# Kernel optimization log

Hardware: AMD Instinct MI355X
Metric: run time of the kernel (lower is better)

Reference implementation:

```python
import jax, jax.numpy as jnp
from jax import lax
import numpy as np

B, T, N = 32, 1024, 128


def setup_inputs() -> dict:
    key = jax.random.key(0)
    k1, k2, k3 = jax.random.split(key, 3)
    x = jax.random.normal(k1, (B, T, N), dtype=jnp.float32)
    w_init = jax.random.normal(k2, (B, N, N), dtype=jnp.float32)
    mask = jax.random.randint(k3, (B, T), 0, 2, dtype=jnp.int32)
    alpha = jnp.float32(0.9)
    eta = jnp.float32(0.01)
    return {"x": x, "w_init": w_init, "alpha": alpha, "eta": eta, "mask": mask}


def reference(x, w_init, alpha, eta, mask):
    # x: (B,T,N), w_init: (B,N,N), mask: (B,T) int {0,1}
    maskf = mask.astype(x.dtype)

    def step(w, inp):
        xt, mt = inp                       # (B,N), (B,)
        yt = jnp.einsum('bij,bj->bi', w, xt)           # read-out with OLD w
        outer = xt[:, :, None] * xt[:, None, :]        # (B,N,N) Hebbian outer product
        w_new = alpha * w + eta * outer                # decay + Hebbian update
        m = mt[:, None, None]
        w = m * w_new + (1.0 - m) * w                  # masked update
        return w, yt

    xs = jnp.swapaxes(x, 0, 1)     # (T,B,N)
    ms = jnp.swapaxes(maskf, 0, 1) # (T,B)
    w_final, ys = lax.scan(step, w_init, (xs, ms))
    y_seq = jnp.swapaxes(ys, 0, 1)  # (B,T,N)
    return w_final, y_seq
```

## Files before the change

### kernel.cpp

```cpp
#include <hip/hip_runtime.h>

#define BB 32
#define TT 1024
#define NN 128
#define YB 256

#define ROR_ADD(p, ctrl)                                                      \
  p += __int_as_float(__builtin_amdgcn_update_dpp(                            \
      0, __float_as_int(p), ctrl, 0xF, 0xF, true));
#define BCAST15_ADD(p)                                                        \
  p += __int_as_float(__builtin_amdgcn_update_dpp(                            \
      0, __float_as_int(p), 0x142, 0xF, 0xF, true));

__global__ __launch_bounds__(256)
void bdh_seq_kernel(const float* __restrict__ x,
                    const float* __restrict__ w_init,
                    const float* __restrict__ alpha_p,
                    const float* __restrict__ eta_p,
                    const int*   __restrict__ mask,
                    float* __restrict__ out)
{
    const int tid  = threadIdx.x;
    const int bidx = blockIdx.x;
    const int b      = bidx & 31;
    const int i_base = (bidx >> 5) << 3;
    const int rloc   = tid >> 5;
    const int i      = i_base + rloc;
    const int cg     = tid & 31;
    const int j0     = cg << 2;

    __shared__ float ybuf[YB][8];

    const float alpha = alpha_p[0];
    const float eta   = eta_p[0];

    const float* xb = x + (size_t)b * TT * NN;
    const int*   mb = mask + b * TT;

    float* wout = out + ((size_t)b * NN + i) * NN + j0;
    float* yout = out + (size_t)BB * NN * NN + (size_t)b * TT * NN;

    float4 w = *reinterpret_cast<const float4*>(
        w_init + ((size_t)b * NN + i) * NN + j0);

    float4 Xc[8], Xn[8];
    float  xic[8], xin[8];
    int    mc[8],  mn[8];
    float  p[16];

#define LOADG(X, XI, M, tbase)                                                \
  {                                                                           \
    const float* gp = xb + (size_t)(tbase) * NN;                              \
    _Pragma("unroll")                                                         \
    for (int k = 0; k < 8; ++k) {                                             \
      X[k]  = *reinterpret_cast<const float4*>(gp + k * NN + j0);             \
      XI[k] = gp[k * NN + i];                                                 \
    }                                                                         \
    *reinterpret_cast<int4*>(&M[0]) =                                         \
        *reinterpret_cast<const int4*>(mb + (tbase));                         \
    *reinterpret_cast<int4*>(&M[4]) =                                         \
        *reinterpret_cast<const int4*>(mb + (tbase) + 4);                     \
  }

#define COMPG(X, XI, M, pbase)                                                \
  {                                                                           \
    _Pragma("unroll")                                                         \
    for (int k = 0; k < 8; ++k) {                                             \
      const float aa = M[k] ? alpha : 1.0f;                                   \
      const float ci = (M[k] ? eta : 0.0f) * XI[k];                           \
      float p0 = fmaf(w.y, X[k].y, w.x * X[k].x);                             \
      float p1 = fmaf(w.w, X[k].w, w.z * X[k].z);                             \
      p[(pbase) + k] = p0 + p1;                                               \
      w.x = fmaf(aa, w.x, ci * X[k].x);                                       \
      w.y = fmaf(aa, w.y, ci * X[k].y);                                       \
      w.z = fmaf(aa, w.z, ci * X[k].z);                                       \
      w.w = fmaf(aa, w.w, ci * X[k].w);                                       \
    }                                                                         \
  }

    LOADG(Xc, xic, mc, 0);
    LOADG(Xn, xin, mn, 8);

#pragma unroll 1
    for (int t = 0; t < TT; t += 16) {
        COMPG(Xc, xic, mc, 0);
        if (t + 16 < TT) LOADG(Xc, xic, mc, t + 16);
        COMPG(Xn, xin, mn, 8);
        if (t + 24 < TT) LOADG(Xn, xin, mn, t + 24);

#pragma unroll
        for (int k = 0; k < 16; ++k) { ROR_ADD(p[k], 0x121); }
#pragma unroll
        for (int k = 0; k < 16; ++k) { ROR_ADD(p[k], 0x122); }
#pragma unroll
        for (int k = 0; k < 16; ++k) { ROR_ADD(p[k], 0x124); }
#pragma unroll
        for (int k = 0; k < 16; ++k) { ROR_ADD(p[k], 0x128); }
#pragma unroll
        for (int k = 0; k < 16; ++k) { BCAST15_ADD(p[k]); }

        if (cg == 16) {
#pragma unroll
            for (int k = 0; k < 16; ++k)
                ybuf[(t + k) & (YB - 1)][rloc] = p[k];
        }

        if (((t + 16) & (YB - 1)) == 0) {
            __syncthreads();
            const int t0 = t + 16 - YB;
#pragma unroll
            for (int pass = 0; pass < 8; ++pass) {
                const int tq = (tid >> 3) + (pass << 5);
                const int il = tid & 7;
                yout[(size_t)(t0 + tq) * NN + i_base + il] = ybuf[tq][il];
            }
            __syncthreads();
        }
    }
#undef LOADG
#undef COMPG

    *reinterpret_cast<float4*>(wout) = w;
}

extern "C" void kernel_launch(void* const* d_in, const int* in_sizes, int n_in,
                              void* d_out, int out_size, void* d_ws, size_t ws_size,
                              hipStream_t stream)
{
    const float* x      = (const float*)d_in[0];
    const float* w_init = (const float*)d_in[1];
    const float* alpha  = (const float*)d_in[2];
    const float* eta    = (const float*)d_in[3];
    const int*   mask   = (const int*)d_in[4];
    float*       out    = (float*)d_out;

    dim3 grid(512), block(256);
    hipLaunchKernelGGL(bdh_seq_kernel, grid, block, 0, stream,
                       x, w_init, alpha, eta, mask, out);
}
```

Measured before the change: 185.1 us.

## Split each W row across a full wavefront with two columns per lane

```diff
diff --git a/kernel.cpp b/kernel.cpp
--- a/kernel.cpp
+++ b/kernel.cpp
@@ -8,11 +8,10 @@
 #define ROR_ADD(p, ctrl)                                                      \
   p += __int_as_float(__builtin_amdgcn_update_dpp(                            \
       0, __float_as_int(p), ctrl, 0xF, 0xF, true));
-#define BCAST15_ADD(p)                                                        \
-  p += __int_as_float(__builtin_amdgcn_update_dpp(                            \
-      0, __float_as_int(p), 0x142, 0xF, 0xF, true));
+#define BCAST15_ADD(p) ROR_ADD(p, 0x142)
+#define BCAST31_ADD(p) ROR_ADD(p, 0x143)
 
-__global__ __launch_bounds__(256)
+__global__ __launch_bounds__(256, 4)
 void bdh_seq_kernel(const float* __restrict__ x,
                     const float* __restrict__ w_init,
                     const float* __restrict__ alpha_p,
@@ -23,13 +22,13 @@
     const int tid  = threadIdx.x;
     const int bidx = blockIdx.x;
     const int b      = bidx & 31;
-    const int i_base = (bidx >> 5) << 3;
-    const int rloc   = tid >> 5;
-    const int i      = i_base + rloc;
-    const int cg     = tid & 31;
-    const int j0     = cg << 2;
+    const int i_base = (bidx >> 5) << 2;
+    const int wv     = tid >> 6;
+    const int lane   = tid & 63;
+    const int i      = i_base + wv;
+    const int j0     = lane << 1;
 
-    __shared__ float ybuf[YB][8];
+    __shared__ float ybuf[YB][4];
 
     const float alpha = alpha_p[0];
     const float eta   = eta_p[0];
@@ -40,10 +39,10 @@
     float* wout = out + ((size_t)b * NN + i) * NN + j0;
     float* yout = out + (size_t)BB * NN * NN + (size_t)b * TT * NN;
 
-    float4 w = *reinterpret_cast<const float4*>(
+    float2 w = *reinterpret_cast<const float2*>(
         w_init + ((size_t)b * NN + i) * NN + j0);
 
-    float4 Xc[8], Xn[8];
+    float2 Xc[8], Xn[8];
     float  xic[8], xin[8];
     int    mc[8],  mn[8];
     float  p[16];
@@ -53,7 +52,7 @@
     const float* gp = xb + (size_t)(tbase) * NN;                              \
     _Pragma("unroll")                                                         \
     for (int k = 0; k < 8; ++k) {                                             \
-      X[k]  = *reinterpret_cast<const float4*>(gp + k * NN + j0);             \
+      X[k]  = *reinterpret_cast<const float2*>(gp + k * NN + j0);             \
       XI[k] = gp[k * NN + i];                                                 \
     }                                                                         \
     *reinterpret_cast<int4*>(&M[0]) =                                         \
@@ -68,13 +67,9 @@
     for (int k = 0; k < 8; ++k) {                                             \
       const float aa = M[k] ? alpha : 1.0f;                                   \
       const float ci = (M[k] ? eta : 0.0f) * XI[k];                           \
-      float p0 = fmaf(w.y, X[k].y, w.x * X[k].x);                             \
-      float p1 = fmaf(w.w, X[k].w, w.z * X[k].z);                             \
-      p[(pbase) + k] = p0 + p1;                                               \
+      p[(pbase) + k] = fmaf(w.y, X[k].y, w.x * X[k].x);                       \
       w.x = fmaf(aa, w.x, ci * X[k].x);                                       \
       w.y = fmaf(aa, w.y, ci * X[k].y);                                       \
-      w.z = fmaf(aa, w.z, ci * X[k].z);                                       \
-      w.w = fmaf(aa, w.w, ci * X[k].w);                                       \
     }                                                                         \
   }
 
@@ -98,20 +93,23 @@
         for (int k = 0; k < 16; ++k) { ROR_ADD(p[k], 0x128); }
 #pragma unroll
         for (int k = 0; k < 16; ++k) { BCAST15_ADD(p[k]); }
+#pragma unroll
+        for (int k = 0; k < 16; ++k) { BCAST31_ADD(p[k]); }
 
-        if (cg == 16) {
+        if (lane == 48) {
 #pragma unroll
             for (int k = 0; k < 16; ++k)
-                ybuf[(t + k) & (YB - 1)][rloc] = p[k];
+                ybuf[(t + k) & (YB - 1)][wv] = p[k];
         }
 
         if (((t + 16) & (YB - 1)) == 0) {
             __syncthreads();
             const int t0 = t + 16 - YB;
 #pragma unroll
-            for (int pass = 0; pass < 8; ++pass) {
-                const int tq = (tid >> 3) + (pass << 5);
-                const int il = tid & 7;
+            for (int pass = 0; pass < 4; ++pass) {
+                const int idx = (pass << 8) + tid;
+                const int tq  = idx >> 2;
+                const int il  = idx & 3;
                 yout[(size_t)(t0 + tq) * NN + i_base + il] = ybuf[tq][il];
             }
             __syncthreads();
@@ -120,7 +118,7 @@
 #undef LOADG
 #undef COMPG
 
-    *reinterpret_cast<float4*>(wout) = w;
+    *reinterpret_cast<float2*>(wout) = w;
 }
 
 extern "C" void kernel_launch(void* const* d_in, const int* in_sizes, int n_in,
@@ -134,7 +132,7 @@
     const int*   mask   = (const int*)d_in[4];
     float*       out    = (float*)d_out;
 
-    dim3 grid(512), block(256);
+    dim3 grid(1024), block(256);
     hipLaunchKernelGGL(bdh_seq_kernel, grid, block, 0, stream,
                        x, w_init, alpha, eta, mask, out);
 }
```

New measurement: 378.1 us. 2.04x slower.
